# Performance work log

Hardware: AMD Instinct MI355X
Metric: run time of the kernel (lower is better)

## Reference

```python
import jax, jax.numpy as jnp
import numpy as np

NUM_HEADS = 4
B, C, N = 2, 128, 4096
NS = N // 2


def setup_inputs() -> dict:
    key = jax.random.key(0)
    ks = jax.random.split(key, 10)
    # idx_select/idx_drop together form a permutation of [0, N) per batch
    perms = jax.vmap(lambda k: jax.random.permutation(k, N))(jax.random.split(ks[8], B))
    idx_select = perms[:, :NS][:, None, :].astype(jnp.int64)
    idx_drop = perms[:, NS:][:, None, :].astype(jnp.int64)
    return {
        "pcd_up": jax.random.normal(ks[0], (B, C, N), jnp.float32),
        "points_select": jax.random.normal(ks[1], (B, C, NS), jnp.float32),
        "points_drop": jax.random.normal(ks[2], (B, C, NS), jnp.float32),
        "pcd_up_xyz": jax.random.normal(ks[3], (B, 3, N), jnp.float32),
        "Wq": jax.random.normal(ks[4], (C, C), jnp.float32) * 0.05,
        "Wk": jax.random.normal(ks[5], (C, C), jnp.float32) * 0.05,
        "Wv": jax.random.normal(ks[6], (C, C), jnp.float32) * 0.05,
        "Wskip": jax.random.normal(ks[7], (C, C), jnp.float32) * 0.05,
        "idx_select": idx_select,
        "idx_drop": idx_drop,
    }


def _concat_by_idx(a, b, idx_a, idx_b):
    # torch: target.scatter(-1, idx, cat([a,b],-1)) with idx expanded over channels
    src = jnp.concatenate([a, b], axis=-1)                  # [B, C, N]
    idx = jnp.concatenate([idx_a, idx_b], axis=-1)[:, 0, :]  # [B, N]
    return jax.vmap(lambda s, i: jnp.zeros_like(s).at[:, i].set(s))(src, idx)


def reference(pcd_up, points_select, points_drop, pcd_up_xyz, Wq, Wk, Wv, Wskip,
              idx_select, idx_drop):
    x = _concat_by_idx(points_select, points_drop, idx_select, idx_drop)  # [B,C,N]
    b, _, n = x.shape

    def proj_split(W, xx):
        y = jnp.einsum('oc,bcn->bon', W, xx)  # 1x1 Conv1d, no bias
        return y.reshape(b, NUM_HEADS, y.shape[1] // NUM_HEADS, n)  # [B,H,D,N]

    q = proj_split(Wq, x)
    k = proj_split(Wk, x)
    v = proj_split(Wv, x)
    dq = q.shape[2]
    # energy = q^T @ k, scaled by sqrt(q_depth)
    energy = jnp.einsum('bhdn,bhdm->bhnm', q, k) / jnp.sqrt(jnp.asarray(dq, x.dtype))
    attn = jax.nn.softmax(energy, axis=-1)                   # [B,H,N,N]
    out = jnp.einsum('bhnm,bhdm->bhnd', attn, v)             # [B,H,N,Dv]
    out = out.transpose(0, 2, 1, 3).reshape(b, n, -1).transpose(0, 2, 1)  # [B,v_out,N]
    return out + jnp.einsum('oc,bcn->bon', Wskip, pcd_up)
```

## Files before the change

### kernel.cpp

```cpp
#include <hip/hip_runtime.h>
#include <cstdint>

#define B_ 2
#define C_ 128
#define N_ 4096
#define H_ 4
#define D_ 32

typedef unsigned short ushort_t;
typedef __attribute__((ext_vector_type(8))) short bf16x8;
typedef __attribute__((ext_vector_type(4))) float f32x4;
typedef __attribute__((ext_vector_type(4))) unsigned int u32x4;

__device__ __forceinline__ ushort_t f2bf(float f) {
  unsigned int u = __builtin_bit_cast(unsigned int, f);
  u += 0x7fffu + ((u >> 16) & 1u);
  return (ushort_t)(u >> 16);
}

__device__ __forceinline__ void stage16(const ushort_t* g, ushort_t* l) {
  __builtin_amdgcn_global_load_lds(
      (const __attribute__((address_space(1))) unsigned int*)g,
      (__attribute__((address_space(3))) unsigned int*)l, 16, 0, 0);
}

__global__ __launch_bounds__(256) void k_prep(const float* __restrict__ psel,
                                              const float* __restrict__ pdrop,
                                              const int* __restrict__ isel,
                                              const int* __restrict__ idrop,
                                              const float* __restrict__ Wq,
                                              const float* __restrict__ Wk,
                                              const float* __restrict__ Wv,
                                              const float* __restrict__ Wsk,
                                              ushort_t* __restrict__ xT,
                                              ushort_t* __restrict__ Wb) {
  int z = blockIdx.z;
  int t = threadIdx.x;
  if (z == 2) {
    int idx = blockIdx.y * 64 + blockIdx.x;
    int m = idx >> 5, sub = idx & 31;
    const float* src = (m == 0) ? Wq : (m == 1) ? Wk : (m == 2) ? Wv : Wsk;
    float sc = (m == 0) ? 0.25506552f : 1.0f;
    int e = sub * 512 + t * 2;
    float2 v = *(const float2*)(src + e);
    unsigned int u = ((unsigned int)f2bf(v.y * sc) << 16) | (unsigned int)f2bf(v.x * sc);
    ((unsigned int*)Wb)[m * 8192 + (e >> 1)] = u;
    return;
  }
  const float* src = z ? pdrop : psel;
  const int* idx = z ? idrop : isel;
  __shared__ ushort_t tile[128][34];
  int b = blockIdx.y;
  int i0 = blockIdx.x * 32;
  {
    int c = t >> 1, ih = (t & 1) * 16;
    const float4* p = (const float4*)(src + ((size_t)(b * 128 + c) * 2048 + i0 + ih));
#pragma unroll
    for (int g = 0; g < 4; ++g) {
      float4 v = p[g];
      tile[c][ih + g * 4 + 0] = f2bf(v.x);
      tile[c][ih + g * 4 + 1] = f2bf(v.y);
      tile[c][ih + g * 4 + 2] = f2bf(v.z);
      tile[c][ih + g * 4 + 3] = f2bf(v.w);
    }
  }
  __syncthreads();
  {
    int i = t >> 3, c0 = (t & 7) * 16;
    int n = idx[b * 2048 + i0 + i];
    alignas(16) ushort_t outv[16];
#pragma unroll
    for (int j = 0; j < 16; ++j) outv[j] = tile[c0 + j][i];
    uint4* q = (uint4*)(xT + ((size_t)(b * 4096 + n) * 128 + c0));
    q[0] = *(uint4*)outv; q[1] = *(uint4*)(outv + 8);
  }
}

__global__ __launch_bounds__(256) void k_proj(const ushort_t* __restrict__ xT,
                                              const float* __restrict__ pcd,
                                              const ushort_t* __restrict__ Wb,
                                              ushort_t* __restrict__ Kb,
                                              ushort_t* __restrict__ Vt,
                                              float* __restrict__ outp) {
  __shared__ ushort_t ldsT[64][136];
  __shared__ float y[128][66];
  int n0 = blockIdx.x * 64, wt = blockIdx.y, b = blockIdx.z, t = threadIdx.x;
  int wave = t >> 6, lane = t & 63, lr = lane & 15, quad = lane >> 4;
  const ushort_t* W = Wb + (size_t)(wt + 1) * 16384;

  if (wt == 2) {
#pragma unroll
    for (int rep = 0; rep < 4; ++rep) {
      int idx = rep * 256 + t;
      int c = idx >> 3, ng = (idx & 7) * 8;
      const float4* p = (const float4*)(pcd + ((size_t)(b * 128 + c) * 4096 + n0 + ng));
      float4 v0 = p[0], v1 = p[1];
      ldsT[ng + 0][c] = f2bf(v0.x); ldsT[ng + 1][c] = f2bf(v0.y);
      ldsT[ng + 2][c] = f2bf(v0.z); ldsT[ng + 3][c] = f2bf(v0.w);
      ldsT[ng + 4][c] = f2bf(v1.x); ldsT[ng + 5][c] = f2bf(v1.y);
      ldsT[ng + 6][c] = f2bf(v1.z); ldsT[ng + 7][c] = f2bf(v1.w);
    }
    __syncthreads();
  }

  f32x4 acc[2][4];
#pragma unroll
  for (int mt = 0; mt < 2; ++mt)
#pragma unroll
    for (int nt = 0; nt < 4; ++nt) acc[mt][nt] = (f32x4){0.f, 0.f, 0.f, 0.f};
#pragma unroll
  for (int kc = 0; kc < 128; kc += 32) {
    bf16x8 a[2], bb[4];
#pragma unroll
    for (int mt = 0; mt < 2; ++mt)
      a[mt] = *(const bf16x8*)(W + (size_t)(wave * 32 + mt * 16 + lr) * 128 + kc + quad * 8);
    if (wt == 2) {
#pragma unroll
      for (int nt = 0; nt < 4; ++nt)
        bb[nt] = *(const bf16x8*)(&ldsT[nt * 16 + lr][kc + quad * 8]);
    } else {
#pragma unroll
      for (int nt = 0; nt < 4; ++nt)
        bb[nt] = *(const bf16x8*)(xT + ((size_t)(b * 4096 + n0 + nt * 16 + lr)) * 128 + kc + quad * 8);
    }
#pragma unroll
    for (int mt = 0; mt < 2; ++mt)
#pragma unroll
      for (int nt = 0; nt < 4; ++nt)
        acc[mt][nt] = __builtin_amdgcn_mfma_f32_16x16x32_bf16(a[mt], bb[nt], acc[mt][nt], 0, 0, 0);
  }

  if (wt == 2) {
#pragma unroll
    for (int mt = 0; mt < 2; ++mt)
#pragma unroll
      for (int nt = 0; nt < 4; ++nt)
#pragma unroll
        for (int r = 0; r < 4; ++r) {
          int o = wave * 32 + mt * 16 + quad * 4 + r;
          outp[(size_t)(b * 128 + o) * 4096 + n0 + nt * 16 + lr] = acc[mt][nt][r];
        }
    return;
  }

#pragma unroll
  for (int mt = 0; mt < 2; ++mt)
#pragma unroll
    for (int nt = 0; nt < 4; ++nt)
#pragma unroll
      for (int r = 0; r < 4; ++r)
        y[wave * 32 + mt * 16 + quad * 4 + r][nt * 16 + lr] = acc[mt][nt][r];
  __syncthreads();

  if (wt == 0) {
    int n = t >> 2, dq = (t & 3) * 8;
#pragma unroll
    for (int h = 0; h < 4; ++h) {
      alignas(16) ushort_t vals[8];
#pragma unroll
      for (int j = 0; j < 8; ++j) vals[j] = f2bf(y[h * 32 + dq + j][n]);
      *(uint4*)(Kb + (((size_t)(b * 4 + h) * 4096 + n0 + n) * 32 + dq)) = *(uint4*)vals;
    }
  } else {
    int o = t >> 1, half = t & 1;
    int h = o >> 5, d = o & 31;
    alignas(16) ushort_t vals[32];
#pragma unroll
    for (int j = 0; j < 32; ++j) {
      int c = half * 32 + ((j >> 3) * 4 + (j & 3) + ((j & 4) << 2));
      vals[j] = f2bf(y[o][c]);
    }
    uint4* dst = (uint4*)(Vt + ((size_t)(b * 4 + h) * 32 + d) * 4096 + n0 + half * 32);
#pragma unroll
    for (int g = 0; g < 4; ++g) dst[g] = *(uint4*)(vals + g * 8);
  }
}

__global__ __launch_bounds__(1024) void k_attn(const ushort_t* __restrict__ xT,
                                               const ushort_t* __restrict__ Wb,
                                               const ushort_t* __restrict__ Kb,
                                               const ushort_t* __restrict__ Vt,
                                               float* __restrict__ outp) {
  __shared__ ushort_t qT[4][32 * 40];
  __shared__ ushort_t stg[4][2][8192];

  int bh = blockIdx.x & 7;
  int q0 = (blockIdx.x >> 3) * 128;
  int b = bh >> 2, h = bh & 3;
  int t = threadIdx.x, wave = t >> 6, lane = t & 63, lr = lane & 15, quad = lane >> 4;
  int qh = wave & 3, kq = wave >> 2, lw = qh;
  int qbase = q0 + qh * 32;
  const ushort_t* xb = xT + (size_t)b * N_ * 128;
  const ushort_t* wqp = Wb + (size_t)h * 32 * 128;
  const ushort_t* Kp = Kb + (size_t)bh * N_ * 32;
  const ushort_t* Vp = Vt + (size_t)bh * 32 * N_;
  const int ks = kq * 1024;

#define STAGE_CHUNK(kcn, buf)                                                          \
  {                                                                                    \
    ushort_t* kb_ = stg[kq][buf];                                                      \
    ushort_t* vb_ = kb_ + 4096;                                                        \
    _Pragma("unroll") for (int j = 0; j < 2; ++j) {                                    \
      int s = lw * 2 + j;                                                              \
      stage16(Kp + (size_t)((kcn) + (s & 1) * 64 + lane) * 32 + (s >> 1) * 8,          \
              kb_ + s * 512);                                                          \
      int I = s * 64 + lane;                                                           \
      stage16(Vp + (size_t)(I & 31) * N_ + (kcn) + ((I >> 5) * 8), vb_ + s * 512);     \
    }                                                                                  \
  }

  if (kq == 0) {
    f32x4 accq[2][2];
#pragma unroll
    for (int mt = 0; mt < 2; ++mt)
#pragma unroll
      for (int nt = 0; nt < 2; ++nt) accq[mt][nt] = (f32x4){0.f, 0.f, 0.f, 0.f};
#pragma unroll
    for (int kc = 0; kc < 128; kc += 32) {
      bf16x8 ax[2], bw[2];
#pragma unroll
      for (int mt = 0; mt < 2; ++mt)
        ax[mt] = *(const bf16x8*)(xb + (size_t)(qbase + mt * 16 + lr) * 128 + kc + quad * 8);
#pragma unroll
      for (int nt = 0; nt < 2; ++nt)
        bw[nt] = *(const bf16x8*)(wqp + (size_t)(nt * 16 + lr) * 128 + kc + quad * 8);
#pragma unroll
      for (int mt = 0; mt < 2; ++mt)
#pragma unroll
        for (int nt = 0; nt < 2; ++nt)
          accq[mt][nt] = __builtin_amdgcn_mfma_f32_16x16x32_bf16(ax[mt], bw[nt], accq[mt][nt], 0, 0, 0);
    }
#pragma unroll
    for (int mt = 0; mt < 2; ++mt)
#pragma unroll
      for (int nt = 0; nt < 2; ++nt)
#pragma unroll
        for (int r = 0; r < 4; ++r)
          qT[qh][(mt * 16 + quad * 4 + r) * 40 + nt * 16 + lr] = f2bf(accq[mt][nt][r]);
  }

  STAGE_CHUNK(ks, 0);
  __syncthreads();

  bf16x8 aq0 = *(const bf16x8*)(&qT[qh][lr * 40 + quad * 8]);
  bf16x8 aq1 = *(const bf16x8*)(&qT[qh][(16 + lr) * 40 + quad * 8]);

  bf16x8 vones;
#pragma unroll
  for (int j = 0; j < 8; ++j) vones[j] = (short)0x3F80;

  f32x4 accO[2][2];
  f32x4 accR[2];
#pragma unroll
  for (int qf = 0; qf < 2; ++qf) {
#pragma unroll
    for (int dt = 0; dt < 2; ++dt) accO[qf][dt] = (f32x4){0.f, 0.f, 0.f, 0.f};
    accR[qf] = (f32x4){0.f, 0.f, 0.f, 0.f};
  }

  for (int it = 0; it < 8; ++it) {
    int cur = it & 1;
    if (it + 1 < 8) STAGE_CHUNK(ks + (it + 1) * 128, cur ^ 1);
    const ushort_t* kb = stg[kq][cur];
    const ushort_t* vb = kb + 4096;
#pragma unroll
    for (int g = 0; g < 4; ++g) {
      bf16x8 bk0 = *(const bf16x8*)(kb + (quad * 128 + g * 32 + lr) * 8);
      bf16x8 bk1 = *(const bf16x8*)(kb + (quad * 128 + g * 32 + 16 + lr) * 8);
      bf16x8 bv0 = *(const bf16x8*)(vb + ((g * 4 + quad) * 32 + lr) * 8);
      bf16x8 bv1 = *(const bf16x8*)(vb + ((g * 4 + quad) * 32 + 16 + lr) * 8);

      f32x4 z = {0.f, 0.f, 0.f, 0.f};
      f32x4 s0 = __builtin_amdgcn_mfma_f32_16x16x32_bf16(bk0, aq0, z, 0, 0, 0);
      f32x4 s1 = __builtin_amdgcn_mfma_f32_16x16x32_bf16(bk1, aq0, z, 0, 0, 0);
      f32x4 s2 = __builtin_amdgcn_mfma_f32_16x16x32_bf16(bk0, aq1, z, 0, 0, 0);
      f32x4 s3 = __builtin_amdgcn_mfma_f32_16x16x32_bf16(bk1, aq1, z, 0, 0, 0);
      float p0[4], p1[4], p2[4], p3[4];
#pragma unroll
      for (int r = 0; r < 4; ++r) {
        p0[r] = __builtin_amdgcn_exp2f(s0[r]);
        p1[r] = __builtin_amdgcn_exp2f(s1[r]);
        p2[r] = __builtin_amdgcn_exp2f(s2[r]);
        p3[r] = __builtin_amdgcn_exp2f(s3[r]);
      }
      u32x4 pk0, pk1;
      pk0.x = __builtin_amdgcn_perm(__builtin_bit_cast(unsigned int, p0[1]),
                                    __builtin_bit_cast(unsigned int, p0[0]), 0x07060302u);
      pk0.y = __builtin_amdgcn_perm(__builtin_bit_cast(unsigned int, p0[3]),
                                    __builtin_bit_cast(unsigned int, p0[2]), 0x07060302u);
      pk0.z = __builtin_amdgcn_perm(__builtin_bit_cast(unsigned int, p1[1]),
                                    __builtin_bit_cast(unsigned int, p1[0]), 0x07060302u);
      pk0.w = __builtin_amdgcn_perm(__builtin_bit_cast(unsigned int, p1[3]),
                                    __builtin_bit_cast(unsigned int, p1[2]), 0x07060302u);
      pk1.x = __builtin_amdgcn_perm(__builtin_bit_cast(unsigned int, p2[1]),
                                    __builtin_bit_cast(unsigned int, p2[0]), 0x07060302u);
      pk1.y = __builtin_amdgcn_perm(__builtin_bit_cast(unsigned int, p2[3]),
                                    __builtin_bit_cast(unsigned int, p2[2]), 0x07060302u);
      pk1.z = __builtin_amdgcn_perm(__builtin_bit_cast(unsigned int, p3[1]),
                                    __builtin_bit_cast(unsigned int, p3[0]), 0x07060302u);
      pk1.w = __builtin_amdgcn_perm(__builtin_bit_cast(unsigned int, p3[3]),
                                    __builtin_bit_cast(unsigned int, p3[2]), 0x07060302u);
      bf16x8 ap0 = __builtin_bit_cast(bf16x8, pk0);
      bf16x8 ap1 = __builtin_bit_cast(bf16x8, pk1);
      accO[0][0] = __builtin_amdgcn_mfma_f32_16x16x32_bf16(ap0, bv0, accO[0][0], 0, 0, 0);
      accO[0][1] = __builtin_amdgcn_mfma_f32_16x16x32_bf16(ap0, bv1, accO[0][1], 0, 0, 0);
      accO[1][0] = __builtin_amdgcn_mfma_f32_16x16x32_bf16(ap1, bv0, accO[1][0], 0, 0, 0);
      accO[1][1] = __builtin_amdgcn_mfma_f32_16x16x32_bf16(ap1, bv1, accO[1][1], 0, 0, 0);
      accR[0] = __builtin_amdgcn_mfma_f32_16x16x32_bf16(ap0, vones, accR[0], 0, 0, 0);
      accR[1] = __builtin_amdgcn_mfma_f32_16x16x32_bf16(ap1, vones, accR[1], 0, 0, 0);
    }
    __syncthreads();
  }

  float* pbuf = (float*)&stg[0][0][0];
  float* obuf = (float*)((char*)&stg[0][0][0] + 98304);

  if (kq != 0) {
    float* pb = pbuf + (((kq - 1) * 4 + qh) * 64 + lane) * 24;
#pragma unroll
    for (int qf = 0; qf < 2; ++qf) {
#pragma unroll
      for (int dt = 0; dt < 2; ++dt)
#pragma unroll
        for (int r = 0; r < 4; ++r) pb[qf * 8 + dt * 4 + r] = accO[qf][dt][r];
#pragma unroll
      for (int r = 0; r < 4; ++r) pb[16 + qf * 4 + r] = accR[qf][r];
    }
  }
  __syncthreads();
  if (kq != 0) return;

#pragma unroll
  for (int j = 0; j < 3; ++j) {
    const float* pb = pbuf + ((j * 4 + qh) * 64 + lane) * 24;
#pragma unroll
    for (int qf = 0; qf < 2; ++qf) {
#pragma unroll
      for (int dt = 0; dt < 2; ++dt)
#pragma unroll
        for (int r = 0; r < 4; ++r) accO[qf][dt][r] += pb[qf * 8 + dt * 4 + r];
#pragma unroll
      for (int r = 0; r < 4; ++r) accR[qf][r] += pb[16 + qf * 4 + r];
    }
  }

  float* ob = obuf + qh * 32 * 33;
#pragma unroll
  for (int qf = 0; qf < 2; ++qf) {
    float rinv[4];
#pragma unroll
    for (int r = 0; r < 4; ++r) rinv[r] = 1.0f / accR[qf][r];
#pragma unroll
    for (int dt = 0; dt < 2; ++dt)
#pragma unroll
      for (int r = 0; r < 4; ++r)
        ob[(dt * 16 + lr) * 33 + qf * 16 + quad * 4 + r] = accO[qf][dt][r] * rinv[r];
  }

  int d = lane >> 1, q16 = (lane & 1) * 16;
  float* po = outp + ((size_t)(b * 128 + h * 32 + d)) * N_ + qbase + q16;
#pragma unroll
  for (int g = 0; g < 4; ++g) {
    float4 r0 = *(float4*)(po + g * 4);
    r0.x += ob[d * 33 + q16 + g * 4 + 0];
    r0.y += ob[d * 33 + q16 + g * 4 + 1];
    r0.z += ob[d * 33 + q16 + g * 4 + 2];
    r0.w += ob[d * 33 + q16 + g * 4 + 3];
    *(float4*)(po + g * 4) = r0;
  }
}

extern "C" void kernel_launch(void* const* d_in, const int* in_sizes, int n_in,
                              void* d_out, int out_size, void* d_ws, size_t ws_size,
                              hipStream_t stream) {
  const float* pcd_up = (const float*)d_in[0];
  const float* psel   = (const float*)d_in[1];
  const float* pdrop  = (const float*)d_in[2];
  const float* Wq  = (const float*)d_in[4];
  const float* Wk  = (const float*)d_in[5];
  const float* Wv  = (const float*)d_in[6];
  const float* Wsk = (const float*)d_in[7];
  const int* isel  = (const int*)d_in[8];
  const int* idrop = (const int*)d_in[9];
  float* out = (float*)d_out;

  ushort_t* xT = (ushort_t*)d_ws;
  ushort_t* Wb = xT + 1048576;
  ushort_t* Kb = Wb + 65536;
  ushort_t* Vt = Kb + 1048576;

  hipLaunchKernelGGL(k_prep, dim3(64, 2, 3), dim3(256), 0, stream,
                     psel, pdrop, isel, idrop, Wq, Wk, Wv, Wsk, xT, Wb);
  hipLaunchKernelGGL(k_proj, dim3(64, 3, 2), dim3(256), 0, stream,
                     xT, pcd_up, Wb, Kb, Vt, out);
  hipLaunchKernelGGL(k_attn, dim3(256), dim3(1024), 0, stream, xT, Wb, Kb, Vt, out);
}
```

Before: 115.6 us.

## Fuse skip projection into attention kernel and merge weight conversion into prep

Moves the Wskip·pcd_up 1x1 projection out of the projection kernel and into the attention kernel. There, the kq==1 waves compute it with MFMA while the first K/V chunk is staged, stage it through LDS and add it in the epilogue. The attention epilogue now writes the output directly instead of reading and then writing it back. Weight bf16 conversion is folded into every prep block rather than a separate grid slice. This removes a global write/read of the output and one grid slice, at the cost of extra work and strided uncoalesced pcd loads inside the attention kernel.

```diff
diff --git a/kernel.cpp b/kernel.cpp
--- a/kernel.cpp
+++ b/kernel.cpp
@@ -35,22 +35,18 @@
                                               ushort_t* __restrict__ xT,
                                               ushort_t* __restrict__ Wb) {
   int z = blockIdx.z;
+  int b = blockIdx.y;
   int t = threadIdx.x;
-  if (z == 2) {
-    int idx = blockIdx.y * 64 + blockIdx.x;
-    int m = idx >> 5, sub = idx & 31;
+  {
+    int gid = (((z * 2 + b) * 64 + blockIdx.x) << 8) + t;
+    int m = gid >> 14, e = gid & 16383;
     const float* src = (m == 0) ? Wq : (m == 1) ? Wk : (m == 2) ? Wv : Wsk;
     float sc = (m == 0) ? 0.25506552f : 1.0f;
-    int e = sub * 512 + t * 2;
-    float2 v = *(const float2*)(src + e);
-    unsigned int u = ((unsigned int)f2bf(v.y * sc) << 16) | (unsigned int)f2bf(v.x * sc);
-    ((unsigned int*)Wb)[m * 8192 + (e >> 1)] = u;
-    return;
+    Wb[m * 16384 + e] = f2bf(src[e] * sc);
   }
   const float* src = z ? pdrop : psel;
   const int* idx = z ? idrop : isel;
   __shared__ ushort_t tile[128][34];
-  int b = blockIdx.y;
   int i0 = blockIdx.x * 32;
   {
     int c = t >> 1, ih = (t & 1) * 16;
@@ -77,32 +73,14 @@
 }
 
 __global__ __launch_bounds__(256) void k_proj(const ushort_t* __restrict__ xT,
-                                              const float* __restrict__ pcd,
                                               const ushort_t* __restrict__ Wb,
                                               ushort_t* __restrict__ Kb,
-                                              ushort_t* __restrict__ Vt,
-                                              float* __restrict__ outp) {
-  __shared__ ushort_t ldsT[64][136];
+                                              ushort_t* __restrict__ Vt) {
   __shared__ float y[128][66];
   int n0 = blockIdx.x * 64, wt = blockIdx.y, b = blockIdx.z, t = threadIdx.x;
   int wave = t >> 6, lane = t & 63, lr = lane & 15, quad = lane >> 4;
   const ushort_t* W = Wb + (size_t)(wt + 1) * 16384;
 
-  if (wt == 2) {
-#pragma unroll
-    for (int rep = 0; rep < 4; ++rep) {
-      int idx = rep * 256 + t;
-      int c = idx >> 3, ng = (idx & 7) * 8;
-      const float4* p = (const float4*)(pcd + ((size_t)(b * 128 + c) * 4096 + n0 + ng));
-      float4 v0 = p[0], v1 = p[1];
-      ldsT[ng + 0][c] = f2bf(v0.x); ldsT[ng + 1][c] = f2bf(v0.y);
-      ldsT[ng + 2][c] = f2bf(v0.z); ldsT[ng + 3][c] = f2bf(v0.w);
-      ldsT[ng + 4][c] = f2bf(v1.x); ldsT[ng + 5][c] = f2bf(v1.y);
-      ldsT[ng + 6][c] = f2bf(v1.z); ldsT[ng + 7][c] = f2bf(v1.w);
-    }
-    __syncthreads();
-  }
-
   f32x4 acc[2][4];
 #pragma unroll
   for (int mt = 0; mt < 2; ++mt)
@@ -114,33 +92,14 @@
 #pragma unroll
     for (int mt = 0; mt < 2; ++mt)
       a[mt] = *(const bf16x8*)(W + (size_t)(wave * 32 + mt * 16 + lr) * 128 + kc + quad * 8);
-    if (wt == 2) {
-#pragma unroll
-      for (int nt = 0; nt < 4; ++nt)
-        bb[nt] = *(const bf16x8*)(&ldsT[nt * 16 + lr][kc + quad * 8]);
-    } else {
-#pragma unroll
-      for (int nt = 0; nt < 4; ++nt)
-        bb[nt] = *(const bf16x8*)(xT + ((size_t)(b * 4096 + n0 + nt * 16 + lr)) * 128 + kc + quad * 8);
-    }
+#pragma unroll
+    for (int nt = 0; nt < 4; ++nt)
+      bb[nt] = *(const bf16x8*)(xT + ((size_t)(b * 4096 + n0 + nt * 16 + lr)) * 128 + kc + quad * 8);
 #pragma unroll
     for (int mt = 0; mt < 2; ++mt)
 #pragma unroll
       for (int nt = 0; nt < 4; ++nt)
         acc[mt][nt] = __builtin_amdgcn_mfma_f32_16x16x32_bf16(a[mt], bb[nt], acc[mt][nt], 0, 0, 0);
-  }
-
-  if (wt == 2) {
-#pragma unroll
-    for (int mt = 0; mt < 2; ++mt)
-#pragma unroll
-      for (int nt = 0; nt < 4; ++nt)
-#pragma unroll
-        for (int r = 0; r < 4; ++r) {
-          int o = wave * 32 + mt * 16 + quad * 4 + r;
-          outp[(size_t)(b * 128 + o) * 4096 + n0 + nt * 16 + lr] = acc[mt][nt][r];
-        }
-    return;
   }
 
 #pragma unroll
@@ -177,6 +136,7 @@
 }
 
 __global__ __launch_bounds__(1024) void k_attn(const ushort_t* __restrict__ xT,
+                                               const float* __restrict__ pcd,
                                                const ushort_t* __restrict__ Wb,
                                                const ushort_t* __restrict__ Kb,
                                                const ushort_t* __restrict__ Vt,
@@ -240,6 +200,35 @@
   }
 
   STAGE_CHUNK(ks, 0);
+
+  f32x4 accS[2][2];
+#pragma unroll
+  for (int mt = 0; mt < 2; ++mt)
+#pragma unroll
+    for (int nt = 0; nt < 2; ++nt) accS[mt][nt] = (f32x4){0.f, 0.f, 0.f, 0.f};
+  if (kq == 1) {
+    const ushort_t* wsk = Wb + 3 * 16384 + (size_t)h * 32 * 128;
+#pragma unroll
+    for (int kc = 0; kc < 128; kc += 32) {
+      bf16x8 aS[2], bW[2];
+#pragma unroll
+      for (int mt = 0; mt < 2; ++mt) {
+        alignas(16) ushort_t tmp[8];
+#pragma unroll
+        for (int j = 0; j < 8; ++j)
+          tmp[j] = f2bf(pcd[((size_t)(b * 128 + kc + quad * 8 + j)) * 4096 + qbase + mt * 16 + lr]);
+        aS[mt] = *(bf16x8*)tmp;
+      }
+#pragma unroll
+      for (int nt = 0; nt < 2; ++nt)
+        bW[nt] = *(const bf16x8*)(wsk + (size_t)(nt * 16 + lr) * 128 + kc + quad * 8);
+#pragma unroll
+      for (int mt = 0; mt < 2; ++mt)
+#pragma unroll
+        for (int nt = 0; nt < 2; ++nt)
+          accS[mt][nt] = __builtin_amdgcn_mfma_f32_16x16x32_bf16(aS[mt], bW[nt], accS[mt][nt], 0, 0, 0);
+    }
+  }
   __syncthreads();
 
   bf16x8 aq0 = *(const bf16x8*)(&qT[qh][lr * 40 + quad * 8]);
@@ -313,7 +302,8 @@
   }
 
   float* pbuf = (float*)&stg[0][0][0];
-  float* obuf = (float*)((char*)&stg[0][0][0] + 98304);
+  float* skipbuf = pbuf + 18432;
+  float* obuf = pbuf + 22528;
 
   if (kq != 0) {
     float* pb = pbuf + (((kq - 1) * 4 + qh) * 64 + lane) * 24;
@@ -326,6 +316,15 @@
 #pragma unroll
       for (int r = 0; r < 4; ++r) pb[16 + qf * 4 + r] = accR[qf][r];
     }
+    if (kq == 1) {
+      float* sb = skipbuf + (qh * 64 + lane) * 16;
+#pragma unroll
+      for (int qf = 0; qf < 2; ++qf)
+#pragma unroll
+        for (int dt = 0; dt < 2; ++dt)
+#pragma unroll
+          for (int r = 0; r < 4; ++r) sb[qf * 8 + dt * 4 + r] = accS[qf][dt][r];
+    }
   }
   __syncthreads();
   if (kq != 0) return;
@@ -344,6 +343,7 @@
     }
   }
 
+  const float* sb = skipbuf + (qh * 64 + lane) * 16;
   float* ob = obuf + qh * 32 * 33;
 #pragma unroll
   for (int qf = 0; qf < 2; ++qf) {
@@ -354,18 +354,19 @@
     for (int dt = 0; dt < 2; ++dt)
 #pragma unroll
       for (int r = 0; r < 4; ++r)
-        ob[(dt * 16 + lr) * 33 + qf * 16 + quad * 4 + r] = accO[qf][dt][r] * rinv[r];
+        ob[(dt * 16 + lr) * 33 + qf * 16 + quad * 4 + r] =
+            accO[qf][dt][r] * rinv[r] + sb[qf * 8 + dt * 4 + r];
   }
 
   int d = lane >> 1, q16 = (lane & 1) * 16;
   float* po = outp + ((size_t)(b * 128 + h * 32 + d)) * N_ + qbase + q16;
 #pragma unroll
   for (int g = 0; g < 4; ++g) {
-    float4 r0 = *(float4*)(po + g * 4);
-    r0.x += ob[d * 33 + q16 + g * 4 + 0];
-    r0.y += ob[d * 33 + q16 + g * 4 + 1];
-    r0.z += ob[d * 33 + q16 + g * 4 + 2];
-    r0.w += ob[d * 33 + q16 + g * 4 + 3];
+    float4 r0;
+    r0.x = ob[d * 33 + q16 + g * 4 + 0];
+    r0.y = ob[d * 33 + q16 + g * 4 + 1];
+    r0.z = ob[d * 33 + q16 + g * 4 + 2];
+    r0.w = ob[d * 33 + q16 + g * 4 + 3];
     *(float4*)(po + g * 4) = r0;
   }
 }
@@ -389,9 +390,9 @@
   ushort_t* Kb = Wb + 65536;
   ushort_t* Vt = Kb + 1048576;
 
-  hipLaunchKernelGGL(k_prep, dim3(64, 2, 3), dim3(256), 0, stream,
+  hipLaunchKernelGGL(k_prep, dim3(64, 2, 2), dim3(256), 0, stream,
                      psel, pdrop, isel, idrop, Wq, Wk, Wv, Wsk, xT, Wb);
-  hipLaunchKernelGGL(k_proj, dim3(64, 3, 2), dim3(256), 0, stream,
+  hipLaunchKernelGGL(k_proj, dim3(64, 2, 2), dim3(256), 0, stream, xT, Wb, Kb, Vt);
+  hipLaunchKernelGGL(k_attn, dim3(256), dim3(1024), 0, stream,
                      xT, pcd_up, Wb, Kb, Vt, out);
-  hipLaunchKernelGGL(k_attn, dim3(256), dim3(1024), 0, stream, xT, Wb, Kb, Vt, out);
-}
+}
```

After: 113.4 us (median of 2 runs). About the same (-1.9%).
